# Optimization experiments

Measured on AMD Instinct MI355X. Metric: run time of the kernel, lower is better.

## Reference

```python
import jax, jax.numpy as jnp
import numpy as np

BS = 131072
NX = 4       # num_dim_x (p, theta, v, omega)
NU = 1       # num_dim_control
H = 256      # n_hidden


def segway_dynamics(x):
    # x: [bs, 4] -> f: [bs, 4], g: [bs, 4, 1]
    theta, v, omega = x[:, 1], x[:, 2], x[:, 3]
    c, s = jnp.cos(theta), jnp.sin(theta)
    f2 = (c * (9.8 * s + 11.5 * v) + 68.4 * v - 1.2 * omega ** 2 * s) / (c - 24.7)
    f3 = (-58.8 * v * c - 243.5 * v - s * (208.3 + omega ** 2 * c)) / (c ** 2 - 24.7)
    f = jnp.stack([v, omega, f2, f3], axis=1)
    g2 = (-1.8 * c - 10.9) / (c - 24.7)
    g3 = (9.3 * c + 38.6) / (c ** 2 - 24.7)
    zero = jnp.zeros_like(g2)
    g = jnp.stack([zero, zero, g2, g3], axis=1)[:, :, None]
    return f, g


def setup_inputs() -> dict:
    key = jax.random.key(0)
    ks = jax.random.split(key, 13)
    d = {"x": jax.random.normal(ks[0], (BS, NX), dtype=jnp.float32)}
    shapes = {
        "Vw1": (H, NX), "Vb1": (H,),
        "Vw2": (H, H),  "Vb2": (H,),
        "Vw3": (H // 4, H), "Vb3": (H // 4,),
        "Uw1": (H, NX), "Ub1": (H,),
        "Uw2": (H, H),  "Ub2": (H,),
        "Uw3": (NU, H), "Ub3": (NU,),
    }
    for i, (name, shp) in enumerate(shapes.items()):
        d[name] = jax.random.normal(ks[i + 1], shp, dtype=jnp.float32) * 0.05
    return d


def reference(x, Vw1, Vb1, Vw2, Vb2, Vw3, Vb3, Uw1, Ub1, Uw2, Ub2, Uw3, Ub3):
    # --- Lyapunov value + analytic gradient ---
    a1 = jnp.tanh(x @ Vw1.T + Vb1)          # [bs, H]
    a2 = jnp.tanh(a1 @ Vw2.T + Vb2)         # [bs, H]
    a3 = jnp.tanh(a2 @ Vw3.T + Vb3)         # [bs, H//4]
    V = 0.5 * jnp.sum(a3 * a3, axis=1)      # [bs]
    # diag_embed(1-tanh^2) @ W  ==  (1-tanh^2)[:, :, None] * W  (no dense diag)
    D1 = (1.0 - a1 ** 2)[:, :, None] * Vw1[None]                          # [bs, H, 4]
    D2 = (1.0 - a2 ** 2)[:, :, None] * jnp.einsum('ij,bjk->bik', Vw2, D1)  # [bs, H, 4]
    D3 = (1.0 - a3 ** 2)[:, :, None] * jnp.einsum('ij,bjk->bik', Vw3, D2)  # [bs, H/4, 4]
    grad_V = jnp.einsum('bi,bij->bj', a3, D3)  # [bs, 4]

    # --- learned controls ---
    u1 = jnp.tanh(x @ Uw1.T + Ub1)
    u2 = jnp.tanh(u1 @ Uw2.T + Ub2)
    u = jnp.tanh(u2 @ Uw3.T + Ub3) * 20.0     # [bs, 1]

    # --- Lie derivatives / Vdot ---
    f, g = segway_dynamics(x)
    L_f_V = jnp.sum(grad_V * f, axis=1, keepdims=True)    # [bs, 1]
    L_g_V = jnp.einsum('bi,bic->bc', grad_V, g)           # [bs, 1]
    Vdot = (L_f_V + jnp.sum(L_g_V * u, axis=1, keepdims=True))[:, :, None]  # [bs,1,1]
    return u, V, Vdot
```

## Files before the change

kernel.cpp:

```cpp
#include <hip/hip_runtime.h>
#include <hip/hip_bf16.h>

#define BSZ 131072

typedef __bf16 v8bf __attribute__((ext_vector_type(8)));
typedef float f32x4 __attribute__((ext_vector_type(4)));

constexpr int RPB = 64;
constexpr int MT  = RPB / 16;
constexpr int NTHREADS = 512;
constexpr int LDA = 264;

constexpr int OFF_B2T = 0;
constexpr int OFF_U2T = 65536;
constexpr int OFF_B2  = 131072;
constexpr int OFF_B3T = 196608;
constexpr int OFF_B3  = 212992;
constexpr int OFF_U3  = 229376;
constexpr int OFF_GV  = 233472;
constexpr int OFF_LV1 = 237568;
constexpr int OFF_LU1 = 245760;
constexpr int WS_ELEMS = 253952;

__device__ __forceinline__ float tanhf_fast(float x){
  float e = __builtin_amdgcn_exp2f(x * 2.885390082f);
  return __builtin_fmaf(-2.0f, __builtin_amdgcn_rcpf(e + 1.0f), 1.0f);
}

__device__ __forceinline__ __bf16 f2bf(float f){
  unsigned u = __builtin_bit_cast(unsigned, f);
  u += 0x8000u;
  unsigned short h = (unsigned short)(u >> 16);
  return __builtin_bit_cast(__bf16, h);
}

__device__ __forceinline__ unsigned pk2bf(float lo, float hi){
  unsigned r;
  asm("v_cvt_pk_bf16_f32 %0, %1, %2" : "=v"(r) : "v"(lo), "v"(hi));
  return r;
}
__device__ __forceinline__ float bflo(unsigned u){ return __builtin_bit_cast(float, u << 16); }
__device__ __forceinline__ float bfhi(unsigned u){ return __builtin_bit_cast(float, u & 0xffff0000u); }

__global__ void prep_weights(const float* __restrict__ Vw2,
                             const float* __restrict__ Uw2,
                             const float* __restrict__ Vw3,
                             const float* __restrict__ Vw1,
                             const float* __restrict__ Uw1,
                             const float* __restrict__ Uw3,
                             __bf16* __restrict__ ws){
  int e = blockIdx.x * 256 + threadIdx.x;
  if (e >= WS_ELEMS) return;
  int idx, NT, base, mode; const float* W;
  if      (e <  65536){ idx = e;          W = Vw2; mode = 0; NT = 16; base = OFF_B2T; }
  else if (e < 131072){ idx = e - 65536;  W = Uw2; mode = 0; NT = 16; base = OFF_U2T; }
  else if (e < 196608){ idx = e - 131072; W = Vw2; mode = 1; NT = 16; base = OFF_B2;  }
  else if (e < 212992){ idx = e - 196608; W = Vw3; mode = 0; NT = 4;  base = OFF_B3T; }
  else if (e < 229376){ idx = e - 212992; W = Vw3; mode = 1; NT = 16; base = OFF_B3;  }
  else if (e < 233472){ idx = e - 229376; W = Uw3; mode = 2; NT = 1;  base = OFF_U3;  }
  else if (e < 237568){ idx = e - 233472; W = Vw1; mode = 3; NT = 1;  base = OFF_GV;  }
  else if (e < 245760){ idx = e - 237568; W = Vw1; mode = 4; NT = 16; base = OFF_LV1; }
  else                { idx = e - 245760; W = Uw1; mode = 4; NT = 16; base = OFF_LU1; }
  int j = idx & 7, l = (idx >> 3) & 63, f = idx >> 9;
  int nt = f % NT, ks = f / NT;
  int k = ks * 32 + (l >> 4) * 8 + j;
  int n = nt * 16 + (l & 15);
  float v;
  if      (mode == 0) v = W[n * 256 + k];
  else if (mode == 1) v = W[k * 256 + n];
  else if (mode == 2) v = (n == 0) ? W[k] : 0.0f;
  else if (mode == 3) v = (n < 4)  ? W[k * 4 + n] : 0.0f;
  else                v = (k < 4)  ? W[n * 4 + k] : 0.0f;
  ws[base + idx] = f2bf(v);
}

__global__ __launch_bounds__(NTHREADS, 4) void fused_clf(
    const float* __restrict__ x, const float* __restrict__ Vw1f,
    const float* __restrict__ Vb1, const float* __restrict__ Vb2,
    const float* __restrict__ Vb3,
    const float* __restrict__ Ub1, const float* __restrict__ Ub2,
    const float* __restrict__ Ub3, const float* __restrict__ Uw3,
    const __bf16* __restrict__ ws,
    float* __restrict__ out)
{
  __shared__ alignas(16) __bf16 b1[RPB][LDA];
  __shared__ alignas(16) __bf16 b2[RPB][LDA];
  __shared__ union alignas(16) S3 {
    __bf16 b3[RPB][72];
    float  r4[8][RPB][4];
  } s3;
  __shared__ alignas(16) float red[RPB][4];
  __shared__ float utile[RPB];

  const int tid  = threadIdx.x;
  const int lane = tid & 63;
  const int wave = tid >> 6;
  const int quad = lane >> 4;
  const int l16  = lane & 15;
  const int row0 = blockIdx.x * RPB;

  uint2 keep_a2[2*MT];

  v8bf xa[MT];
  #pragma unroll
  for (int m = 0; m < MT; m++){
    v8bf z;
    #pragma unroll
    for (int j = 0; j < 8; j++) z[j] = (__bf16)0.0f;
    if (quad == 0){
      float4 xv = ((const float4*)x)[row0 + m*16 + l16];
      z[0] = f2bf(xv.x); z[1] = f2bf(xv.y); z[2] = f2bf(xv.z); z[3] = f2bf(xv.w);
    }
    xa[m] = z;
  }


  auto layer1m = [&](const __bf16* __restrict__ Bw, const float* __restrict__ bv,
                     __bf16 (*dst)[LDA]){
    const v8bf* B = (const v8bf*)Bw;
    v8bf bf0 = B[(wave*2 + 0)*64 + lane];
    v8bf bf1 = B[(wave*2 + 1)*64 + lane];
    f32x4 acc[MT][2];
    #pragma unroll
    for (int m = 0; m < MT; m++){ f32x4 z={0.f,0.f,0.f,0.f}; acc[m][0]=z; acc[m][1]=z; }
    __builtin_amdgcn_s_setprio(1);
    #pragma unroll
    for (int m = 0; m < MT; m++){
      acc[m][0] = __builtin_amdgcn_mfma_f32_16x16x32_bf16(bf0, xa[m], acc[m][0], 0,0,0);
      acc[m][1] = __builtin_amdgcn_mfma_f32_16x16x32_bf16(bf1, xa[m], acc[m][1], 0,0,0);
    }
    __builtin_amdgcn_s_setprio(0);
    #pragma unroll
    for (int nt = 0; nt < 2; nt++){
      const int f0 = (wave*2 + nt)*16 + quad*4;
      f32x4 bvv = ((const f32x4*)bv)[f0 >> 2];
      #pragma unroll
      for (int m = 0; m < MT; m++){
        const int brow = m*16 + l16;
        uint2 pk;
        pk.x = pk2bf(tanhf_fast(acc[m][nt][0] + bvv[0]),
                     tanhf_fast(acc[m][nt][1] + bvv[1]));
        pk.y = pk2bf(tanhf_fast(acc[m][nt][2] + bvv[2]),
                     tanhf_fast(acc[m][nt][3] + bvv[3]));
        *(uint2*)&dst[brow][f0] = pk;
      }
    }
  };

  auto gemm256t = [&](const __bf16 (*A)[LDA], const __bf16* __restrict__ Bw,
                      const float* __restrict__ bias, __bf16 (*dst)[LDA],
                      uint2* keep){
    f32x4 acc[MT][2];
    #pragma unroll
    for (int m = 0; m < MT; m++){ f32x4 z={0.f,0.f,0.f,0.f}; acc[m][0]=z; acc[m][1]=z; }
    const v8bf* B = (const v8bf*)Bw;
    __builtin_amdgcn_s_setprio(1);
    #pragma unroll
    for (int kk = 0; kk < 8; kk++){
      v8bf a[MT];
      #pragma unroll
      for (int m = 0; m < MT; m++)
        a[m] = *(const v8bf*)&A[m*16 + l16][kk*32 + quad*8];
      #pragma unroll
      for (int nt = 0; nt < 2; nt++){
        v8bf bf = B[(kk*16 + wave*2 + nt)*64 + lane];
        #pragma unroll
        for (int m = 0; m < MT; m++)
          acc[m][nt] = __builtin_amdgcn_mfma_f32_16x16x32_bf16(bf, a[m], acc[m][nt], 0,0,0);
      }
    }
    __builtin_amdgcn_s_setprio(0);
    #pragma unroll
    for (int nt = 0; nt < 2; nt++){
      const int f0 = (wave*2 + nt)*16 + quad*4;
      f32x4 bvv = ((const f32x4*)bias)[f0 >> 2];
      #pragma unroll
      for (int m = 0; m < MT; m++){
        const int brow = m*16 + l16;
        uint2 pk;
        pk.x = pk2bf(tanhf_fast(acc[m][nt][0] + bvv[0]),
                     tanhf_fast(acc[m][nt][1] + bvv[1]));
        pk.y = pk2bf(tanhf_fast(acc[m][nt][2] + bvv[2]),
                     tanhf_fast(acc[m][nt][3] + bvv[3]));
        if (keep) keep[nt*MT + m] = pk;
        *(uint2*)&dst[brow][f0] = pk;
      }
    }
  };

  auto u2dot = [&](const __bf16 (*A)[LDA], const __bf16* __restrict__ Bw,
                   const float* __restrict__ bias, const float* __restrict__ w3){
    f32x4 acc[MT][2];
    #pragma unroll
    for (int m = 0; m < MT; m++){ f32x4 z={0.f,0.f,0.f,0.f}; acc[m][0]=z; acc[m][1]=z; }
    const v8bf* B = (const v8bf*)Bw;
    __builtin_amdgcn_s_setprio(1);
    #pragma unroll
    for (int kk = 0; kk < 8; kk++){
      v8bf a[MT];
      #pragma unroll
      for (int m = 0; m < MT; m++)
        a[m] = *(const v8bf*)&A[m*16 + l16][kk*32 + quad*8];
      #pragma unroll
      for (int nt = 0; nt < 2; nt++){
        v8bf bf = B[(kk*16 + wave*2 + nt)*64 + lane];
        #pragma unroll
        for (int m = 0; m < MT; m++)
          acc[m][nt] = __builtin_amdgcn_mfma_f32_16x16x32_bf16(bf, a[m], acc[m][nt], 0,0,0);
      }
    }
    __builtin_amdgcn_s_setprio(0);
    float part[MT];
    #pragma unroll
    for (int m = 0; m < MT; m++) part[m] = 0.f;
    #pragma unroll
    for (int nt = 0; nt < 2; nt++){
      const int f0 = (wave*2 + nt)*16 + quad*4;
      f32x4 bvv = ((const f32x4*)bias)[f0 >> 2];
      f32x4 w3v = ((const f32x4*)w3)[f0 >> 2];
      #pragma unroll
      for (int m = 0; m < MT; m++)
        #pragma unroll
        for (int r = 0; r < 4; r++)
          part[m] = __builtin_fmaf(tanhf_fast(acc[m][nt][r] + bvv[r]), w3v[r], part[m]);
    }
    #pragma unroll
    for (int m = 0; m < MT; m++){
      part[m] += __shfl_xor(part[m], 16);
      part[m] += __shfl_xor(part[m], 32);
    }
    if (quad == 0){
      #pragma unroll
      for (int m = 0; m < MT; m++)
        s3.r4[wave][m*16 + l16][0] = part[m];
    }
  };

  layer1m(ws + OFF_LU1, Ub1, b2);
  layer1m(ws + OFF_LV1, Vb1, b1);
  __syncthreads();
  u2dot(b2, ws + OFF_U2T, Ub2, Uw3);
  __syncthreads();
  gemm256t(b1, ws + OFF_B2T, Vb2, b2, keep_a2);
  if (tid < RPB){
    float z = Ub3[0];
    #pragma unroll
    for (int w = 0; w < 8; w++) z += s3.r4[w][tid][0];
    float u = tanhf_fast(z) * 20.0f;
    utile[tid] = u;
    out[row0 + tid] = u;
  }
  __syncthreads();

  {
    const int mp = wave >> 2;
    const int nt = wave & 3;
    f32x4 acc[2];
    { f32x4 z={0.f,0.f,0.f,0.f}; acc[0]=z; acc[1]=z; }
    const v8bf* B = (const v8bf*)(ws + OFF_B3T);
    __builtin_amdgcn_s_setprio(1);
    #pragma unroll
    for (int kk = 0; kk < 8; kk++){
      v8bf bf = B[(kk*4 + nt)*64 + lane];
      #pragma unroll
      for (int m2 = 0; m2 < 2; m2++){
        v8bf a = *(const v8bf*)&b2[(mp*2 + m2)*16 + l16][kk*32 + quad*8];
        acc[m2] = __builtin_amdgcn_mfma_f32_16x16x32_bf16(bf, a, acc[m2], 0,0,0);
      }
    }
    __builtin_amdgcn_s_setprio(0);
    const int f0 = nt*16 + quad*4;
    f32x4 bvv = ((const f32x4*)Vb3)[f0 >> 2];
    #pragma unroll
    for (int m2 = 0; m2 < 2; m2++){
      const int brow = (mp*2 + m2)*16 + l16;
      float t0 = tanhf_fast(acc[m2][0] + bvv[0]);
      float t1 = tanhf_fast(acc[m2][1] + bvv[1]);
      float t2 = tanhf_fast(acc[m2][2] + bvv[2]);
      float t3 = tanhf_fast(acc[m2][3] + bvv[3]);
      float s0 = t0*t0, s1 = t1*t1, s2 = t2*t2, s3q = t3*t3;
      float sq = (s0 + s1) + (s2 + s3q);
      sq += __shfl_xor(sq, 16);
      sq += __shfl_xor(sq, 32);
      if (quad == 0) red[brow][nt] = sq;
      uint2 pk;
      pk.x = pk2bf(t0*(1.0f - s0), t1*(1.0f - s1));
      pk.y = pk2bf(t2*(1.0f - s2), t3*(1.0f - s3q));
      *(uint2*)&s3.b3[brow][f0] = pk;
    }
  }
  __syncthreads();

  {
    f32x4 acc[MT][2];
    #pragma unroll
    for (int m = 0; m < MT; m++){ f32x4 z={0.f,0.f,0.f,0.f}; acc[m][0]=z; acc[m][1]=z; }
    const v8bf* B = (const v8bf*)(ws + OFF_B3);
    __builtin_amdgcn_s_setprio(1);
    #pragma unroll
    for (int kk = 0; kk < 2; kk++){
      v8bf a[MT];
      #pragma unroll
      for (int m = 0; m < MT; m++)
        a[m] = *(const v8bf*)&s3.b3[m*16 + l16][kk*32 + quad*8];
      #pragma unroll
      for (int nt = 0; nt < 2; nt++){
        v8bf bf = B[(kk*16 + wave*2 + nt)*64 + lane];
        #pragma unroll
        for (int m = 0; m < MT; m++)
          acc[m][nt] = __builtin_amdgcn_mfma_f32_16x16x32_bf16(bf, a[m], acc[m][nt], 0,0,0);
      }
    }
    __builtin_amdgcn_s_setprio(0);
    #pragma unroll
    for (int nt = 0; nt < 2; nt++){
      const int f0 = (wave*2 + nt)*16 + quad*4;
      #pragma unroll
      for (int m = 0; m < MT; m++){
        const int brow = m*16 + l16;
        uint2 old = keep_a2[nt*MT + m];
        float a0 = bflo(old.x), a1 = bfhi(old.x);
        float c0 = bflo(old.y), c1 = bfhi(old.y);
        uint2 pk;
        pk.x = pk2bf(acc[m][nt][0] * (1.0f - a0*a0),
                     acc[m][nt][1] * (1.0f - a1*a1));
        pk.y = pk2bf(acc[m][nt][2] * (1.0f - c0*c0),
                     acc[m][nt][3] * (1.0f - c1*c1));
        *(uint2*)&b2[brow][f0] = pk;
      }
    }
    if (tid < RPB)
      out[BSZ + row0 + tid] = 0.5f * (red[tid][0] + red[tid][1] + red[tid][2] + red[tid][3]);
  }
  __syncthreads();

  {
    f32x4 acc[MT][2];
    #pragma unroll
    for (int m = 0; m < MT; m++){ f32x4 z={0.f,0.f,0.f,0.f}; acc[m][0]=z; acc[m][1]=z; }
    const v8bf* B = (const v8bf*)(ws + OFF_B2);
    __builtin_amdgcn_s_setprio(1);
    #pragma unroll
    for (int kk = 0; kk < 8; kk++){
      v8bf a[MT];
      #pragma unroll
      for (int m = 0; m < MT; m++)
        a[m] = *(const v8bf*)&b2[m*16 + l16][kk*32 + quad*8];
      #pragma unroll
      for (int nt = 0; nt < 2; nt++){
        v8bf bf = B[(kk*16 + wave*2 + nt)*64 + lane];
        #pragma unroll
        for (int m = 0; m < MT; m++)
          acc[m][nt] = __builtin_amdgcn_mfma_f32_16x16x32_bf16(bf, a[m], acc[m][nt], 0,0,0);
      }
    }
    __builtin_amdgcn_s_setprio(0);
    f32x4 gp[MT];
    #pragma unroll
    for (int m = 0; m < MT; m++){ f32x4 z={0.f,0.f,0.f,0.f}; gp[m]=z; }
    #pragma unroll
    for (int nt = 0; nt < 2; nt++){
      const int f0 = (wave*2 + nt)*16 + quad*4;
      f32x4 vw0 = ((const f32x4*)Vw1f)[f0 + 0];
      f32x4 vw1 = ((const f32x4*)Vw1f)[f0 + 1];
      f32x4 vw2 = ((const f32x4*)Vw1f)[f0 + 2];
      f32x4 vw3 = ((const f32x4*)Vw1f)[f0 + 3];
      #pragma unroll
      for (int m = 0; m < MT; m++){
        uint2 old = *(const uint2*)&b1[m*16 + l16][f0];
        float a0 = bflo(old.x), a1 = bfhi(old.x);
        float c0 = bflo(old.y), c1 = bfhi(old.y);
        float s0 = acc[m][nt][0] * (1.0f - a0*a0);
        float s1 = acc[m][nt][1] * (1.0f - a1*a1);
        float s2 = acc[m][nt][2] * (1.0f - c0*c0);
        float s3v = acc[m][nt][3] * (1.0f - c1*c1);
        gp[m] += s0*vw0 + s1*vw1 + s2*vw2 + s3v*vw3;
      }
    }
    #pragma unroll
    for (int m = 0; m < MT; m++){
      #pragma unroll
      for (int j = 0; j < 4; j++){
        float v = gp[m][j];
        v += __shfl_xor(v, 16);
        v += __shfl_xor(v, 32);
        gp[m][j] = v;
      }
      if (quad == 0)
        *(f32x4*)&s3.r4[wave][m*16 + l16][0] = gp[m];
    }
  }
  __syncthreads();
  if (tid < RPB*4){
    int b = tid >> 2, k2 = tid & 3;
    float s = 0.f;
    #pragma unroll
    for (int w = 0; w < 8; w++) s += s3.r4[w][b][k2];
    red[b][k2] = s;
  }
  __syncthreads();

  if (tid < RPB){
    float4 xv = ((const float4*)x)[row0 + tid];
    float th = xv.y, vv = xv.z, om = xv.w;
    float c, s;
    __sincosf(th, &s, &c);
    float rdc  = __builtin_amdgcn_rcpf(c - 24.7f);
    float rdc2 = __builtin_amdgcn_rcpf(c*c - 24.7f);
    float f2v = (c*(9.8f*s + 11.5f*vv) + 68.4f*vv - 1.2f*om*om*s) * rdc;
    float f3v = (-58.8f*vv*c - 243.5f*vv - s*(208.3f + om*om*c)) * rdc2;
    float g2v = (-1.8f*c - 10.9f) * rdc;
    float g3v = (9.3f*c + 38.6f) * rdc2;
    f32x4 rv = *(const f32x4*)&red[tid][0];
    float Lf = rv[0]*vv + rv[1]*om + rv[2]*f2v + rv[3]*f3v;
    float Lg = rv[2]*g2v + rv[3]*g3v;
    out[2*BSZ + row0 + tid] = Lf + Lg * utile[tid];
  }
}

extern "C" void kernel_launch(void* const* d_in, const int* in_sizes, int n_in,
                              void* d_out, int out_size, void* d_ws, size_t ws_size,
                              hipStream_t stream) {
  const float* x   = (const float*)d_in[0];
  const float* Vw1 = (const float*)d_in[1];
  const float* Vb1 = (const float*)d_in[2];
  const float* Vw2 = (const float*)d_in[3];
  const float* Vb2 = (const float*)d_in[4];
  const float* Vw3 = (const float*)d_in[5];
  const float* Vb3 = (const float*)d_in[6];
  const float* Uw1 = (const float*)d_in[7];
  const float* Ub1 = (const float*)d_in[8];
  const float* Uw2 = (const float*)d_in[9];
  const float* Ub2 = (const float*)d_in[10];
  const float* Uw3 = (const float*)d_in[11];
  const float* Ub3 = (const float*)d_in[12];
  __bf16* ws = (__bf16*)d_ws;
  float* out = (float*)d_out;

  hipLaunchKernelGGL(prep_weights, dim3((WS_ELEMS + 255) / 256), dim3(256), 0, stream,
                     Vw2, Uw2, Vw3, Vw1, Uw1, Uw3, ws);
  hipLaunchKernelGGL(fused_clf, dim3(BSZ / RPB), dim3(NTHREADS), 0, stream,
                     x, Vw1, Vb1, Vb2, Vb3, Ub1, Ub2, Ub3, Uw3, ws, out);
}
```

Baseline: 166.1 us.

## Merge two LDS activation buffers into one and raise occupancy target

Replaces the two 64x264 bf16 shared buffers with a single buffer. Layer-1 activations of the V network are kept in registers (keep_a1) instead of shared memory, and the U and V stages are reordered so the buffer can be reused, with an extra barrier added before overwriting it in layer 2. Launch bounds rise from 4 to 6 blocks per multiprocessor to exploit the smaller LDS footprint. The trade-offs are more register pressure, extra synchronisation and a serialised U/V layer-1 schedule.

```diff
diff --git a/kernel.cpp b/kernel.cpp
--- a/kernel.cpp
+++ b/kernel.cpp
@@ -74,7 +74,7 @@
   ws[base + idx] = f2bf(v);
 }
 
-__global__ __launch_bounds__(NTHREADS, 4) void fused_clf(
+__global__ __launch_bounds__(NTHREADS, 6) void fused_clf(
     const float* __restrict__ x, const float* __restrict__ Vw1f,
     const float* __restrict__ Vb1, const float* __restrict__ Vb2,
     const float* __restrict__ Vb3,
@@ -83,8 +83,7 @@
     const __bf16* __restrict__ ws,
     float* __restrict__ out)
 {
-  __shared__ alignas(16) __bf16 b1[RPB][LDA];
-  __shared__ alignas(16) __bf16 b2[RPB][LDA];
+  __shared__ alignas(16) __bf16 buf[RPB][LDA];
   __shared__ union alignas(16) S3 {
     __bf16 b3[RPB][72];
     float  r4[8][RPB][4];
@@ -99,6 +98,7 @@
   const int l16  = lane & 15;
   const int row0 = blockIdx.x * RPB;
 
+  uint2 keep_a1[2*MT];
   uint2 keep_a2[2*MT];
 
   v8bf xa[MT];
@@ -116,7 +116,7 @@
 
 
   auto layer1m = [&](const __bf16* __restrict__ Bw, const float* __restrict__ bv,
-                     __bf16 (*dst)[LDA]){
+                     uint2* keep){
     const v8bf* B = (const v8bf*)Bw;
     v8bf bf0 = B[(wave*2 + 0)*64 + lane];
     v8bf bf1 = B[(wave*2 + 1)*64 + lane];
@@ -134,46 +134,6 @@
     for (int nt = 0; nt < 2; nt++){
       const int f0 = (wave*2 + nt)*16 + quad*4;
       f32x4 bvv = ((const f32x4*)bv)[f0 >> 2];
-      #pragma unroll
-      for (int m = 0; m < MT; m++){
-        const int brow = m*16 + l16;
-        uint2 pk;
-        pk.x = pk2bf(tanhf_fast(acc[m][nt][0] + bvv[0]),
-                     tanhf_fast(acc[m][nt][1] + bvv[1]));
-        pk.y = pk2bf(tanhf_fast(acc[m][nt][2] + bvv[2]),
-                     tanhf_fast(acc[m][nt][3] + bvv[3]));
-        *(uint2*)&dst[brow][f0] = pk;
-      }
-    }
-  };
-
-  auto gemm256t = [&](const __bf16 (*A)[LDA], const __bf16* __restrict__ Bw,
-                      const float* __restrict__ bias, __bf16 (*dst)[LDA],
-                      uint2* keep){
-    f32x4 acc[MT][2];
-    #pragma unroll
-    for (int m = 0; m < MT; m++){ f32x4 z={0.f,0.f,0.f,0.f}; acc[m][0]=z; acc[m][1]=z; }
-    const v8bf* B = (const v8bf*)Bw;
-    __builtin_amdgcn_s_setprio(1);
-    #pragma unroll
-    for (int kk = 0; kk < 8; kk++){
-      v8bf a[MT];
-      #pragma unroll
-      for (int m = 0; m < MT; m++)
-        a[m] = *(const v8bf*)&A[m*16 + l16][kk*32 + quad*8];
-      #pragma unroll
-      for (int nt = 0; nt < 2; nt++){
-        v8bf bf = B[(kk*16 + wave*2 + nt)*64 + lane];
-        #pragma unroll
-        for (int m = 0; m < MT; m++)
-          acc[m][nt] = __builtin_amdgcn_mfma_f32_16x16x32_bf16(bf, a[m], acc[m][nt], 0,0,0);
-      }
-    }
-    __builtin_amdgcn_s_setprio(0);
-    #pragma unroll
-    for (int nt = 0; nt < 2; nt++){
-      const int f0 = (wave*2 + nt)*16 + quad*4;
-      f32x4 bvv = ((const f32x4*)bias)[f0 >> 2];
       #pragma unroll
       for (int m = 0; m < MT; m++){
         const int brow = m*16 + l16;
@@ -183,12 +143,12 @@
         pk.y = pk2bf(tanhf_fast(acc[m][nt][2] + bvv[2]),
                      tanhf_fast(acc[m][nt][3] + bvv[3]));
         if (keep) keep[nt*MT + m] = pk;
-        *(uint2*)&dst[brow][f0] = pk;
+        *(uint2*)&buf[brow][f0] = pk;
       }
     }
   };
 
-  auto u2dot = [&](const __bf16 (*A)[LDA], const __bf16* __restrict__ Bw,
+  auto u2dot = [&](const __bf16* __restrict__ Bw,
                    const float* __restrict__ bias, const float* __restrict__ w3){
     f32x4 acc[MT][2];
     #pragma unroll
@@ -200,7 +160,7 @@
       v8bf a[MT];
       #pragma unroll
       for (int m = 0; m < MT; m++)
-        a[m] = *(const v8bf*)&A[m*16 + l16][kk*32 + quad*8];
+        a[m] = *(const v8bf*)&buf[m*16 + l16][kk*32 + quad*8];
       #pragma unroll
       for (int nt = 0; nt < 2; nt++){
         v8bf bf = B[(kk*16 + wave*2 + nt)*64 + lane];
@@ -236,12 +196,11 @@
     }
   };
 
-  layer1m(ws + OFF_LU1, Ub1, b2);
-  layer1m(ws + OFF_LV1, Vb1, b1);
-  __syncthreads();
-  u2dot(b2, ws + OFF_U2T, Ub2, Uw3);
-  __syncthreads();
-  gemm256t(b1, ws + OFF_B2T, Vb2, b2, keep_a2);
+  layer1m(ws + OFF_LU1, Ub1, nullptr);
+  __syncthreads();
+  u2dot(ws + OFF_U2T, Ub2, Uw3);
+  __syncthreads();
+  layer1m(ws + OFF_LV1, Vb1, keep_a1);
   if (tid < RPB){
     float z = Ub3[0];
     #pragma unroll
@@ -249,6 +208,47 @@
     float u = tanhf_fast(z) * 20.0f;
     utile[tid] = u;
     out[row0 + tid] = u;
+  }
+  __syncthreads();
+
+  {
+    f32x4 acc[MT][2];
+    #pragma unroll
+    for (int m = 0; m < MT; m++){ f32x4 z={0.f,0.f,0.f,0.f}; acc[m][0]=z; acc[m][1]=z; }
+    const v8bf* B = (const v8bf*)(ws + OFF_B2T);
+    __builtin_amdgcn_s_setprio(1);
+    #pragma unroll
+    for (int kk = 0; kk < 8; kk++){
+      v8bf a[MT];
+      #pragma unroll
+      for (int m = 0; m < MT; m++)
+        a[m] = *(const v8bf*)&buf[m*16 + l16][kk*32 + quad*8];
+      #pragma unroll
+      for (int nt = 0; nt < 2; nt++){
+        v8bf bf = B[(kk*16 + wave*2 + nt)*64 + lane];
+        #pragma unroll
+        for (int m = 0; m < MT; m++)
+          acc[m][nt] = __builtin_amdgcn_mfma_f32_16x16x32_bf16(bf, a[m], acc[m][nt], 0,0,0);
+      }
+    }
+    __builtin_amdgcn_s_setprio(0);
+    __syncthreads();
+    #pragma unroll
+    for (int nt = 0; nt < 2; nt++){
+      const int f0 = (wave*2 + nt)*16 + quad*4;
+      f32x4 bvv = ((const f32x4*)Vb2)[f0 >> 2];
+      #pragma unroll
+      for (int m = 0; m < MT; m++){
+        const int brow = m*16 + l16;
+        uint2 pk;
+        pk.x = pk2bf(tanhf_fast(acc[m][nt][0] + bvv[0]),
+                     tanhf_fast(acc[m][nt][1] + bvv[1]));
+        pk.y = pk2bf(tanhf_fast(acc[m][nt][2] + bvv[2]),
+                     tanhf_fast(acc[m][nt][3] + bvv[3]));
+        keep_a2[nt*MT + m] = pk;
+        *(uint2*)&buf[brow][f0] = pk;
+      }
+    }
   }
   __syncthreads();
 
@@ -264,7 +264,7 @@
       v8bf bf = B[(kk*4 + nt)*64 + lane];
       #pragma unroll
       for (int m2 = 0; m2 < 2; m2++){
-        v8bf a = *(const v8bf*)&b2[(mp*2 + m2)*16 + l16][kk*32 + quad*8];
+        v8bf a = *(const v8bf*)&buf[(mp*2 + m2)*16 + l16][kk*32 + quad*8];
         acc[m2] = __builtin_amdgcn_mfma_f32_16x16x32_bf16(bf, a, acc[m2], 0,0,0);
       }
     }
@@ -326,7 +326,7 @@
                      acc[m][nt][1] * (1.0f - a1*a1));
         pk.y = pk2bf(acc[m][nt][2] * (1.0f - c0*c0),
                      acc[m][nt][3] * (1.0f - c1*c1));
-        *(uint2*)&b2[brow][f0] = pk;
+        *(uint2*)&buf[brow][f0] = pk;
       }
     }
     if (tid < RPB)
@@ -345,7 +345,7 @@
       v8bf a[MT];
       #pragma unroll
       for (int m = 0; m < MT; m++)
-        a[m] = *(const v8bf*)&b2[m*16 + l16][kk*32 + quad*8];
+        a[m] = *(const v8bf*)&buf[m*16 + l16][kk*32 + quad*8];
       #pragma unroll
       for (int nt = 0; nt < 2; nt++){
         v8bf bf = B[(kk*16 + wave*2 + nt)*64 + lane];
@@ -367,7 +367,7 @@
       f32x4 vw3 = ((const f32x4*)Vw1f)[f0 + 3];
       #pragma unroll
       for (int m = 0; m < MT; m++){
-        uint2 old = *(const uint2*)&b1[m*16 + l16][f0];
+        uint2 old = keep_a1[nt*MT + m];
         float a0 = bflo(old.x), a1 = bfhi(old.x);
         float c0 = bflo(old.y), c1 = bfhi(old.y);
         float s0 = acc[m][nt][0] * (1.0f - a0*a0);
```

Measured after the change: 215.2 us. 29.5% more time.

## Run U and V second-layer GEMMs concurrently on split wave groups

Applied to the files above, without the earlier changes.

Instead of running the U-network layer-2 GEMM and then the V-network layer-2 GEMM sequentially across all 8 waves, waves 0-3 compute the U GEMM while waves 4-7 compute the V GEMM, each wave taking 4 N-tiles. This removes one barrier-separated phase and lets both GEMMs share the same A-fragment loop. The a2 activations are no longer kept in registers; the later derivative step re-reads them from shared memory, trading register pressure for an extra LDS read. Accumulator count per wave doubles, which may raise register use and affect occupancy.

```diff
diff --git a/kernel.cpp b/kernel.cpp
--- a/kernel.cpp
+++ b/kernel.cpp
@@ -91,6 +91,7 @@
   } s3;
   __shared__ alignas(16) float red[RPB][4];
   __shared__ float utile[RPB];
+  __shared__ float upart[4][RPB];
 
   const int tid  = threadIdx.x;
   const int lane = tid & 63;
@@ -98,8 +99,6 @@
   const int quad = lane >> 4;
   const int l16  = lane & 15;
   const int row0 = blockIdx.x * RPB;
-
-  uint2 keep_a2[2*MT];
 
   v8bf xa[MT];
   #pragma unroll
@@ -147,13 +146,20 @@
     }
   };
 
-  auto gemm256t = [&](const __bf16 (*A)[LDA], const __bf16* __restrict__ Bw,
-                      const float* __restrict__ bias, __bf16 (*dst)[LDA],
-                      uint2* keep){
-    f32x4 acc[MT][2];
-    #pragma unroll
-    for (int m = 0; m < MT; m++){ f32x4 z={0.f,0.f,0.f,0.f}; acc[m][0]=z; acc[m][1]=z; }
-    const v8bf* B = (const v8bf*)Bw;
+  layer1m(ws + OFF_LU1, Ub1, b2);
+  layer1m(ws + OFF_LV1, Vb1, b1);
+  __syncthreads();
+
+  {
+    const int grp = wave >> 2;
+    const int w4  = wave & 3;
+    const __bf16 (*A)[LDA] = grp ? b1 : b2;
+    const v8bf* B = (const v8bf*)(ws + (grp ? OFF_B2T : OFF_U2T));
+    f32x4 acc[MT][4];
+    #pragma unroll
+    for (int m = 0; m < MT; m++)
+      #pragma unroll
+      for (int j = 0; j < 4; j++){ f32x4 z={0.f,0.f,0.f,0.f}; acc[m][j]=z; }
     __builtin_amdgcn_s_setprio(1);
     #pragma unroll
     for (int kk = 0; kk < 8; kk++){
@@ -162,96 +168,63 @@
       for (int m = 0; m < MT; m++)
         a[m] = *(const v8bf*)&A[m*16 + l16][kk*32 + quad*8];
       #pragma unroll
-      for (int nt = 0; nt < 2; nt++){
-        v8bf bf = B[(kk*16 + wave*2 + nt)*64 + lane];
+      for (int j = 0; j < 4; j++){
+        v8bf bf = B[(kk*16 + w4*4 + j)*64 + lane];
         #pragma unroll
         for (int m = 0; m < MT; m++)
-          acc[m][nt] = __builtin_amdgcn_mfma_f32_16x16x32_bf16(bf, a[m], acc[m][nt], 0,0,0);
+          acc[m][j] = __builtin_amdgcn_mfma_f32_16x16x32_bf16(bf, a[m], acc[m][j], 0,0,0);
       }
     }
     __builtin_amdgcn_s_setprio(0);
-    #pragma unroll
-    for (int nt = 0; nt < 2; nt++){
-      const int f0 = (wave*2 + nt)*16 + quad*4;
-      f32x4 bvv = ((const f32x4*)bias)[f0 >> 2];
-      #pragma unroll
-      for (int m = 0; m < MT; m++){
-        const int brow = m*16 + l16;
-        uint2 pk;
-        pk.x = pk2bf(tanhf_fast(acc[m][nt][0] + bvv[0]),
-                     tanhf_fast(acc[m][nt][1] + bvv[1]));
-        pk.y = pk2bf(tanhf_fast(acc[m][nt][2] + bvv[2]),
-                     tanhf_fast(acc[m][nt][3] + bvv[3]));
-        if (keep) keep[nt*MT + m] = pk;
-        *(uint2*)&dst[brow][f0] = pk;
-      }
-    }
-  };
-
-  auto u2dot = [&](const __bf16 (*A)[LDA], const __bf16* __restrict__ Bw,
-                   const float* __restrict__ bias, const float* __restrict__ w3){
-    f32x4 acc[MT][2];
-    #pragma unroll
-    for (int m = 0; m < MT; m++){ f32x4 z={0.f,0.f,0.f,0.f}; acc[m][0]=z; acc[m][1]=z; }
-    const v8bf* B = (const v8bf*)Bw;
-    __builtin_amdgcn_s_setprio(1);
-    #pragma unroll
-    for (int kk = 0; kk < 8; kk++){
-      v8bf a[MT];
-      #pragma unroll
-      for (int m = 0; m < MT; m++)
-        a[m] = *(const v8bf*)&A[m*16 + l16][kk*32 + quad*8];
-      #pragma unroll
-      for (int nt = 0; nt < 2; nt++){
-        v8bf bf = B[(kk*16 + wave*2 + nt)*64 + lane];
+    __syncthreads();
+    if (grp == 0){
+      float part[MT];
+      #pragma unroll
+      for (int m = 0; m < MT; m++) part[m] = 0.f;
+      #pragma unroll
+      for (int j = 0; j < 4; j++){
+        const int f0 = (w4*4 + j)*16 + quad*4;
+        f32x4 bvv = ((const f32x4*)Ub2)[f0 >> 2];
+        f32x4 w3v = ((const f32x4*)Uw3)[f0 >> 2];
         #pragma unroll
         for (int m = 0; m < MT; m++)
-          acc[m][nt] = __builtin_amdgcn_mfma_f32_16x16x32_bf16(bf, a[m], acc[m][nt], 0,0,0);
-      }
-    }
-    __builtin_amdgcn_s_setprio(0);
-    float part[MT];
-    #pragma unroll
-    for (int m = 0; m < MT; m++) part[m] = 0.f;
-    #pragma unroll
-    for (int nt = 0; nt < 2; nt++){
-      const int f0 = (wave*2 + nt)*16 + quad*4;
-      f32x4 bvv = ((const f32x4*)bias)[f0 >> 2];
-      f32x4 w3v = ((const f32x4*)w3)[f0 >> 2];
-      #pragma unroll
-      for (int m = 0; m < MT; m++)
+          #pragma unroll
+          for (int r = 0; r < 4; r++)
+            part[m] = __builtin_fmaf(tanhf_fast(acc[m][j][r] + bvv[r]), w3v[r], part[m]);
+      }
+      #pragma unroll
+      for (int m = 0; m < MT; m++){
+        part[m] += __shfl_xor(part[m], 16);
+        part[m] += __shfl_xor(part[m], 32);
+        if (quad == 0) upart[w4][m*16 + l16] = part[m];
+      }
+    } else {
+      #pragma unroll
+      for (int j = 0; j < 4; j++){
+        const int f0 = (w4*4 + j)*16 + quad*4;
+        f32x4 bvv = ((const f32x4*)Vb2)[f0 >> 2];
         #pragma unroll
-        for (int r = 0; r < 4; r++)
-          part[m] = __builtin_fmaf(tanhf_fast(acc[m][nt][r] + bvv[r]), w3v[r], part[m]);
-    }
-    #pragma unroll
-    for (int m = 0; m < MT; m++){
-      part[m] += __shfl_xor(part[m], 16);
-      part[m] += __shfl_xor(part[m], 32);
-    }
-    if (quad == 0){
-      #pragma unroll
-      for (int m = 0; m < MT; m++)
-        s3.r4[wave][m*16 + l16][0] = part[m];
-    }
-  };
-
-  layer1m(ws + OFF_LU1, Ub1, b2);
-  layer1m(ws + OFF_LV1, Vb1, b1);
-  __syncthreads();
-  u2dot(b2, ws + OFF_U2T, Ub2, Uw3);
-  __syncthreads();
-  gemm256t(b1, ws + OFF_B2T, Vb2, b2, keep_a2);
+        for (int m = 0; m < MT; m++){
+          uint2 pk;
+          pk.x = pk2bf(tanhf_fast(acc[m][j][0] + bvv[0]),
+                       tanhf_fast(acc[m][j][1] + bvv[1]));
+          pk.y = pk2bf(tanhf_fast(acc[m][j][2] + bvv[2]),
+                       tanhf_fast(acc[m][j][3] + bvv[3]));
+          *(uint2*)&b2[m*16 + l16][f0] = pk;
+        }
+      }
+    }
+  }
+  __syncthreads();
+
   if (tid < RPB){
     float z = Ub3[0];
     #pragma unroll
-    for (int w = 0; w < 8; w++) z += s3.r4[w][tid][0];
+    for (int w = 0; w < 4; w++) z += upart[w][tid];
     float u = tanhf_fast(z) * 20.0f;
     utile[tid] = u;
     out[row0 + tid] = u;
   }
-  __syncthreads();
-
   {
     const int mp = wave >> 2;
     const int nt = wave & 3;
@@ -318,7 +291,7 @@
       #pragma unroll
       for (int m = 0; m < MT; m++){
         const int brow = m*16 + l16;
-        uint2 old = keep_a2[nt*MT + m];
+        uint2 old = *(const uint2*)&b2[brow][f0];
         float a0 = bflo(old.x), a1 = bfhi(old.x);
         float c0 = bflo(old.y), c1 = bfhi(old.y);
         uint2 pk;
```

New measurement: 171.9 us. 3.5% more time.
